# Optimization experiments

Measured on AMD Instinct MI355X. Metric: run time of the kernel, lower is better.

## Reference

```python
import jax, jax.numpy as jnp
import numpy as np

B, I, N = 1024, 128, 256
UNFOLDS = 6  # ode_solver_unfolds


def _sig(v, mu, sigma):
    # v: [B, D] -> [B, D, 1]; mu/sigma: [D, N] -> broadcast [B, D, N]
    return jax.nn.sigmoid(sigma * (v[..., None] - mu))


def setup_inputs() -> dict:
    key = jax.random.key(0)
    ks = jax.random.split(key, 12)
    u = lambda k, shape, lo, hi: jax.random.uniform(k, shape, jnp.float32, lo, hi)
    pm1 = lambda k, shape: (2.0 * jax.random.randint(k, shape, 0, 2) - 1.0).astype(jnp.float32)
    return {
        "inputs": jax.random.normal(ks[0], (B, I), jnp.float32),
        "state": jax.random.normal(ks[1], (B, N), jnp.float32) * 0.1,
        "input_w": jnp.ones((I,), jnp.float32),
        "input_b": jnp.zeros((I,), jnp.float32),
        "sensory_mu": u(ks[2], (I, N), 0.3, 0.8),
        "sensory_sigma": u(ks[3], (I, N), 3.0, 8.0),
        "sensory_W": u(ks[4], (I, N), 0.01, 1.0),
        "sensory_erev": pm1(ks[5], (I, N)),
        "mu": u(ks[6], (N, N), 0.3, 0.8),
        "sigma": u(ks[7], (N, N), 3.0, 8.0),
        "W": u(ks[8], (N, N), 0.01, 1.0),
        "erev": pm1(ks[9], (N, N)),
        "vleak": u(ks[10], (N,), -0.2, 0.2),
        "gleak": jnp.ones((N,), jnp.float32),   # gleak_init_min == gleak_init_max == 1.0
        "cm_t": jnp.full((N,), 0.5, jnp.float32),  # cm_init_min == cm_init_max == 0.5
    }


def reference(inputs, state, input_w, input_b, sensory_mu, sensory_sigma,
              sensory_W, sensory_erev, mu, sigma, W, erev, vleak, gleak, cm_t):
    # Affine input mapping
    x = inputs * input_w + input_b  # [B, I]
    # Sensory synapse activations (constant across unfolds)
    s_act = sensory_W * _sig(x, sensory_mu, sensory_sigma)  # [B, I, N]
    w_num_sensory = jnp.sum(s_act * sensory_erev, axis=1)   # [B, N]
    w_den_sensory = jnp.sum(s_act, axis=1)                  # [B, N]

    def step(v_pre, _):
        w_act = W * _sig(v_pre, mu, sigma)                  # [B, N, N]
        w_num = jnp.sum(w_act * erev, axis=1) + w_num_sensory
        w_den = jnp.sum(w_act, axis=1) + w_den_sensory
        numerator = cm_t * v_pre + gleak * vleak + w_num
        denominator = cm_t + gleak + w_den
        return numerator / denominator, None

    v_pre, _ = jax.lax.scan(step, state, None, length=UNFOLDS)
    # module returns (outputs, next_state) with outputs == next_state
    return v_pre
```

## Files before the change

### kernel.cpp

```cpp
#include <hip/hip_runtime.h>


#define LOG2E 1.44269504088896340f

constexpr int Bn = 1024;
constexpr int In = 128;
constexpr int Nn = 256;
constexpr int UNFOLDS = 6;

#if __has_builtin(__builtin_amdgcn_exp2f)
#define EXP2F(x) __builtin_amdgcn_exp2f(x)
#else
#define EXP2F(x) __exp2f(x)
#endif
#if __has_builtin(__builtin_amdgcn_rcpf)
#define RCPF(x) __builtin_amdgcn_rcpf(x)
#else
#define RCPF(x) (1.0f / (x))
#endif

__global__ __launch_bounds__(256) void pack_kernel(
    const float* __restrict__ mu, const float* __restrict__ sigma,
    const float* __restrict__ W, const float* __restrict__ erev,
    const float* __restrict__ smu, const float* __restrict__ ssigma,
    const float* __restrict__ sW, const float* __restrict__ serev,
    float4* __restrict__ Prec, float4* __restrict__ Psen) {
    int idx = blockIdx.x * 256 + threadIdx.x;
    if (idx < Nn * Nn) {
        float s = sigma[idx], m = mu[idx], w = W[idx], e = erev[idx];
        Prec[idx] = make_float4(s * LOG2E, s * m * LOG2E, w, w * e);
        return;
    }
    int j = idx - Nn * Nn;
    if (j < In * Nn) {
        float s = ssigma[j], m = smu[j], w = sW[j], e = serev[j];
        Psen[j] = make_float4(s * LOG2E, s * m * LOG2E, w, w * e);
    }
}

__global__ __launch_bounds__(1024, 1) void ltc_fused_kernel(
    const float* __restrict__ inputs, const float* __restrict__ state,
    const float* __restrict__ input_w, const float* __restrict__ input_b,
    const float4* __restrict__ Psen, const float4* __restrict__ Prec,
    const float* __restrict__ vleak, const float* __restrict__ gleak,
    const float* __restrict__ cmt, float* __restrict__ out) {
    __shared__ float4 vt[Nn];
    __shared__ float2 part[4][4][Nn];
    __shared__ float4 xs[In];

    const int tid = threadIdx.x;
    const int b0 = blockIdx.x * 4;
    const int n = tid & 255;
    const int ih = tid >> 8;

    float vp = state[(b0 + ih) * Nn + n];
    ((float*)vt)[n * 4 + ih] = vp;
    if (tid < 4 * In) {
        int i = tid & 127, bb = tid >> 7;
        ((float*)xs)[i * 4 + bb] =
            inputs[(b0 + bb) * In + i] * input_w[i] + input_b[i];
    }
    const float g = gleak[n], c = cmt[n];
    const float gvl = g * vleak[n];
    __syncthreads();

    float sens_n, sens_d;
    {
        float num[4] = {0.f, 0.f, 0.f, 0.f};
        float den[4] = {0.f, 0.f, 0.f, 0.f};
        const float4* __restrict__ pp = Psen + n;
#pragma unroll 8
        for (int i = ih * 32; i < ih * 32 + 32; ++i) {
            float4 p = pp[i * Nn];
            float4 v = xs[i];
#pragma unroll
            for (int bb = 0; bb < 4; ++bb) {
                float vb = (bb == 0) ? v.x : (bb == 1) ? v.y : (bb == 2) ? v.z : v.w;
                float r = RCPF(1.0f + EXP2F(fmaf(-p.x, vb, p.y)));
                den[bb] += p.z * r;
                num[bb] += p.w * r;
            }
        }
#pragma unroll
        for (int bb = 0; bb < 4; ++bb)
            part[ih][bb][n] = make_float2(num[bb], den[bb]);
        __syncthreads();
        float wn = 0.f, wd = 0.f;
#pragma unroll
        for (int s = 0; s < 4; ++s) {
            float2 v = part[s][ih][n];
            wn += v.x;
            wd += v.y;
        }
        sens_n = wn;
        sens_d = wd;
    }

    const float4* __restrict__ pp = Prec + n;
    for (int s = 0; s < UNFOLDS; ++s) {
        __syncthreads();
        float num[4] = {0.f, 0.f, 0.f, 0.f};
        float den[4] = {0.f, 0.f, 0.f, 0.f};
#pragma unroll 8
        for (int i = ih * 64; i < ih * 64 + 64; ++i) {
            float4 p = pp[i * Nn];
            float4 v = vt[i];
#pragma unroll
            for (int bb = 0; bb < 4; ++bb) {
                float vb = (bb == 0) ? v.x : (bb == 1) ? v.y : (bb == 2) ? v.z : v.w;
                float r = RCPF(1.0f + EXP2F(fmaf(-p.x, vb, p.y)));
                den[bb] += p.z * r;
                num[bb] += p.w * r;
            }
        }
#pragma unroll
        for (int bb = 0; bb < 4; ++bb)
            part[ih][bb][n] = make_float2(num[bb], den[bb]);
        __syncthreads();
        float wn = sens_n, wd = sens_d;
#pragma unroll
        for (int s2 = 0; s2 < 4; ++s2) {
            float2 v = part[s2][ih][n];
            wn += v.x;
            wd += v.y;
        }
        float res = (c * vp + gvl + wn) * RCPF(c + g + wd);
        vp = res;
        if (s == UNFOLDS - 1)
            out[(b0 + ih) * Nn + n] = res;
        else
            ((float*)vt)[n * 4 + ih] = res;
    }
}

extern "C" void kernel_launch(void* const* d_in, const int* in_sizes, int n_in,
                              void* d_out, int out_size, void* d_ws, size_t ws_size,
                              hipStream_t stream) {
    const float* inputs   = (const float*)d_in[0];
    const float* state    = (const float*)d_in[1];
    const float* input_w  = (const float*)d_in[2];
    const float* input_b  = (const float*)d_in[3];
    const float* smu      = (const float*)d_in[4];
    const float* ssigma   = (const float*)d_in[5];
    const float* sW       = (const float*)d_in[6];
    const float* serev    = (const float*)d_in[7];
    const float* mu       = (const float*)d_in[8];
    const float* sigma    = (const float*)d_in[9];
    const float* W        = (const float*)d_in[10];
    const float* erev     = (const float*)d_in[11];
    const float* vleak    = (const float*)d_in[12];
    const float* gleak    = (const float*)d_in[13];
    const float* cmt      = (const float*)d_in[14];
    float* out = (float*)d_out;

    char* ws = (char*)d_ws;
    float4* Prec = (float4*)ws;
    float4* Psen = (float4*)(ws + (1u << 20));

    pack_kernel<<<(Nn * Nn + In * Nn + 255) / 256, 256, 0, stream>>>(
        mu, sigma, W, erev, smu, ssigma, sW, serev, Prec, Psen);

    ltc_fused_kernel<<<Bn / 4, 1024, 0, stream>>>(
        inputs, state, input_w, input_b, Psen, Prec, vleak, gleak, cmt, out);
}
```

Baseline: 180.7 us.

## Split each batch group across two blocks with global-memory state exchange

Each group of 4 batch rows is now handled by a pair of blocks, each owning half of the 256 output neurons, which doubles the grid to 512 blocks so more of the GPU's compute units are busy. After every unfold the two blocks swap their updated state through a global buffer and sync on a per-pair atomic counter with spin-waiting. This adds inter-block dependencies that could deadlock if paired blocks are not resident together, which the spin bound only limits, and it adds global-memory round trips at each step. It also adds a memset launch.

```diff
diff --git a/kernel.cpp b/kernel.cpp
--- a/kernel.cpp
+++ b/kernel.cpp
@@ -38,39 +38,52 @@
     }
 }
 
-__global__ __launch_bounds__(1024, 1) void ltc_fused_kernel(
+__global__ __launch_bounds__(1024, 8) void ltc_fused_kernel(
     const float* __restrict__ inputs, const float* __restrict__ state,
     const float* __restrict__ input_w, const float* __restrict__ input_b,
     const float4* __restrict__ Psen, const float4* __restrict__ Prec,
     const float* __restrict__ vleak, const float* __restrict__ gleak,
-    const float* __restrict__ cmt, float* __restrict__ out) {
+    const float* __restrict__ cmt, float* __restrict__ out,
+    float* __restrict__ xchg, int* __restrict__ flags) {
     __shared__ float4 vt[Nn];
-    __shared__ float2 part[4][4][Nn];
     __shared__ float4 xs[In];
-
-    const int tid = threadIdx.x;
-    const int b0 = blockIdx.x * 4;
-    const int n = tid & 255;
-    const int ih = tid >> 8;
-
-    float vp = state[(b0 + ih) * Nn + n];
-    ((float*)vt)[n * 4 + ih] = vp;
-    if (tid < 4 * In) {
+    __shared__ float2 part[8][4][128];
+
+    const int tid    = threadIdx.x;
+    const int blk    = blockIdx.x;
+    const int pairid = blk >> 1;
+    const int nh     = blk & 1;
+    const int b0     = pairid * 4;
+    const int nl     = tid & 127;
+    const int ih     = tid >> 7;
+    const int ng     = (nh << 7) + nl;
+
+    {
+        int i = tid & 255, bb = tid >> 8;
+        ((float*)vt)[i * 4 + bb] = state[(b0 + bb) * Nn + i];
+    }
+    if (tid < 512) {
         int i = tid & 127, bb = tid >> 7;
         ((float*)xs)[i * 4 + bb] =
             inputs[(b0 + bb) * In + i] * input_w[i] + input_b[i];
     }
-    const float g = gleak[n], c = cmt[n];
-    const float gvl = g * vleak[n];
+    const bool is_red = (ih < 4);
+    float vp = 0.f, g = 0.f, c = 0.f, gvl = 0.f;
+    if (is_red) {
+        g   = gleak[ng];
+        c   = cmt[ng];
+        gvl = g * vleak[ng];
+    }
     __syncthreads();
-
-    float sens_n, sens_d;
+    if (is_red) vp = ((const float*)vt)[ng * 4 + ih];
+
+    float sens_n = 0.f, sens_d = 0.f;
     {
         float num[4] = {0.f, 0.f, 0.f, 0.f};
         float den[4] = {0.f, 0.f, 0.f, 0.f};
-        const float4* __restrict__ pp = Psen + n;
+        const float4* __restrict__ pp = Psen + ng;
 #pragma unroll 8
-        for (int i = ih * 32; i < ih * 32 + 32; ++i) {
+        for (int i = ih * 16; i < ih * 16 + 16; ++i) {
             float4 p = pp[i * Nn];
             float4 v = xs[i];
 #pragma unroll
@@ -83,26 +96,25 @@
         }
 #pragma unroll
         for (int bb = 0; bb < 4; ++bb)
-            part[ih][bb][n] = make_float2(num[bb], den[bb]);
+            part[ih][bb][nl] = make_float2(num[bb], den[bb]);
         __syncthreads();
-        float wn = 0.f, wd = 0.f;
-#pragma unroll
-        for (int s = 0; s < 4; ++s) {
-            float2 v = part[s][ih][n];
-            wn += v.x;
-            wd += v.y;
-        }
-        sens_n = wn;
-        sens_d = wd;
-    }
-
-    const float4* __restrict__ pp = Prec + n;
-    for (int s = 0; s < UNFOLDS; ++s) {
+        if (is_red) {
+#pragma unroll
+            for (int s = 0; s < 8; ++s) {
+                float2 v = part[s][ih][nl];
+                sens_n += v.x;
+                sens_d += v.y;
+            }
+        }
+    }
+
+    const float4* __restrict__ pp = Prec + ng;
+    for (int u = 0; u < UNFOLDS; ++u) {
         __syncthreads();
         float num[4] = {0.f, 0.f, 0.f, 0.f};
         float den[4] = {0.f, 0.f, 0.f, 0.f};
 #pragma unroll 8
-        for (int i = ih * 64; i < ih * 64 + 64; ++i) {
+        for (int i = ih * 32; i < ih * 32 + 32; ++i) {
             float4 p = pp[i * Nn];
             float4 v = vt[i];
 #pragma unroll
@@ -115,21 +127,50 @@
         }
 #pragma unroll
         for (int bb = 0; bb < 4; ++bb)
-            part[ih][bb][n] = make_float2(num[bb], den[bb]);
+            part[ih][bb][nl] = make_float2(num[bb], den[bb]);
         __syncthreads();
-        float wn = sens_n, wd = sens_d;
-#pragma unroll
-        for (int s2 = 0; s2 < 4; ++s2) {
-            float2 v = part[s2][ih][n];
-            wn += v.x;
-            wd += v.y;
-        }
-        float res = (c * vp + gvl + wn) * RCPF(c + g + wd);
-        vp = res;
-        if (s == UNFOLDS - 1)
-            out[(b0 + ih) * Nn + n] = res;
-        else
-            ((float*)vt)[n * 4 + ih] = res;
+
+        if (is_red) {
+            float wn = sens_n, wd = sens_d;
+#pragma unroll
+            for (int s = 0; s < 8; ++s) {
+                float2 v = part[s][ih][nl];
+                wn += v.x;
+                wd += v.y;
+            }
+            float res = (c * vp + gvl + wn) * RCPF(c + g + wd);
+            vp = res;
+            if (u == UNFOLDS - 1) {
+                out[(b0 + ih) * Nn + ng] = res;
+            } else {
+                ((float*)vt)[ng * 4 + ih] = res;
+                __hip_atomic_store(
+                    &xchg[(((u & 1) << 9) + blk) * 512 + (nl << 2) + ih], res,
+                    __ATOMIC_RELAXED, __HIP_MEMORY_SCOPE_AGENT);
+            }
+        }
+
+        if (u < UNFOLDS - 1) {
+            __syncthreads();
+            if (tid == 0) {
+                __hip_atomic_fetch_add(&flags[pairid], 1, __ATOMIC_RELAXED,
+                                       __HIP_MEMORY_SCOPE_AGENT);
+                const int target = 2 * (u + 1);
+                int it = 0;
+                while (__hip_atomic_load(&flags[pairid], __ATOMIC_RELAXED,
+                                         __HIP_MEMORY_SCOPE_AGENT) < target) {
+                    __builtin_amdgcn_s_sleep(2);
+                    if (++it > (1 << 20)) break;
+                }
+            }
+            __syncthreads();
+            if (tid < 512) {
+                float pv = __hip_atomic_load(
+                    &xchg[(((u & 1) << 9) + (blk ^ 1)) * 512 + tid],
+                    __ATOMIC_RELAXED, __HIP_MEMORY_SCOPE_AGENT);
+                ((float*)vt)[((1 - nh) << 9) + tid] = pv;
+            }
+        }
     }
 }
 
@@ -156,10 +197,15 @@
     char* ws = (char*)d_ws;
     float4* Prec = (float4*)ws;
     float4* Psen = (float4*)(ws + (1u << 20));
+    float*  xchg = (float*)(ws + (1u << 20) + (1u << 19));
+    int*    flags = (int*)(ws + (1u << 20) + (1u << 19) + (2u << 20));
+
+    hipMemsetAsync(flags, 0, 256 * sizeof(int), stream);
 
     pack_kernel<<<(Nn * Nn + In * Nn + 255) / 256, 256, 0, stream>>>(
         mu, sigma, W, erev, smu, ssigma, sW, serev, Prec, Psen);
 
-    ltc_fused_kernel<<<Bn / 4, 1024, 0, stream>>>(
-        inputs, state, input_w, input_b, Psen, Prec, vleak, gleak, cmt, out);
+    ltc_fused_kernel<<<dim3(Bn / 4 * 2), dim3(1024), 0, stream>>>(
+        inputs, state, input_w, input_b, Psen, Prec, vleak, gleak, cmt, out,
+        xchg, flags);
 }
```

Result: slower. 211.4 us (+17.0%).

## Pack W and W*erev as bf16 pair and use 2-batch blocks

Applied to the files above, without the earlier changes.

Stores the synapse weight and weight*erev pair as two bf16 halves in one 32-bit word, splitting the parameter layout into a float2 array for the sigmoid coefficients and a uint array for the weights. This cuts parameter bytes per synapse from 16 to 12. The fused kernel now processes 2 batch rows per 512-thread block with up to 4 blocks per CU instead of 4 rows per 1024-thread block. That raises block count and occupancy but halves the reuse of each loaded parameter across batch rows. Rounding the weights to bf16 introduces precision loss in the accumulated sums.

```diff
diff --git a/kernel.cpp b/kernel.cpp
--- a/kernel.cpp
+++ b/kernel.cpp
@@ -19,45 +19,57 @@
 #define RCPF(x) (1.0f / (x))
 #endif
 
+__device__ __forceinline__ unsigned int pack_bf16_pair(float w, float we) {
+    unsigned int uw = __float_as_uint(w);
+    unsigned int ue = __float_as_uint(we);
+    uw = (uw + 0x7fffu + ((uw >> 16) & 1u)) & 0xffff0000u;
+    ue = (ue + 0x7fffu + ((ue >> 16) & 1u)) >> 16;
+    return uw | ue;
+}
+
 __global__ __launch_bounds__(256) void pack_kernel(
     const float* __restrict__ mu, const float* __restrict__ sigma,
     const float* __restrict__ W, const float* __restrict__ erev,
     const float* __restrict__ smu, const float* __restrict__ ssigma,
     const float* __restrict__ sW, const float* __restrict__ serev,
-    float4* __restrict__ Prec, float4* __restrict__ Psen) {
+    float2* __restrict__ PAB, unsigned int* __restrict__ PWE,
+    float2* __restrict__ SAB, unsigned int* __restrict__ SWE) {
     int idx = blockIdx.x * 256 + threadIdx.x;
     if (idx < Nn * Nn) {
         float s = sigma[idx], m = mu[idx], w = W[idx], e = erev[idx];
-        Prec[idx] = make_float4(s * LOG2E, s * m * LOG2E, w, w * e);
+        PAB[idx] = make_float2(s * LOG2E, s * m * LOG2E);
+        PWE[idx] = pack_bf16_pair(w, w * e);
         return;
     }
     int j = idx - Nn * Nn;
     if (j < In * Nn) {
         float s = ssigma[j], m = smu[j], w = sW[j], e = serev[j];
-        Psen[j] = make_float4(s * LOG2E, s * m * LOG2E, w, w * e);
+        SAB[j] = make_float2(s * LOG2E, s * m * LOG2E);
+        SWE[j] = pack_bf16_pair(w, w * e);
     }
 }
 
-__global__ __launch_bounds__(1024, 1) void ltc_fused_kernel(
+__global__ __launch_bounds__(512, 4) void ltc_fused_kernel(
     const float* __restrict__ inputs, const float* __restrict__ state,
     const float* __restrict__ input_w, const float* __restrict__ input_b,
-    const float4* __restrict__ Psen, const float4* __restrict__ Prec,
+    const float2* __restrict__ SAB, const unsigned int* __restrict__ SWE,
+    const float2* __restrict__ PAB, const unsigned int* __restrict__ PWE,
     const float* __restrict__ vleak, const float* __restrict__ gleak,
     const float* __restrict__ cmt, float* __restrict__ out) {
-    __shared__ float4 vt[Nn];
-    __shared__ float2 part[4][4][Nn];
-    __shared__ float4 xs[In];
+    __shared__ float2 vt[Nn];
+    __shared__ float2 xs[In];
+    __shared__ float2 part[2][2][Nn];
 
     const int tid = threadIdx.x;
-    const int b0 = blockIdx.x * 4;
+    const int b0 = blockIdx.x * 2;
     const int n = tid & 255;
     const int ih = tid >> 8;
 
     float vp = state[(b0 + ih) * Nn + n];
-    ((float*)vt)[n * 4 + ih] = vp;
-    if (tid < 4 * In) {
+    ((float*)vt)[n * 2 + ih] = vp;
+    if (tid < 2 * In) {
         int i = tid & 127, bb = tid >> 7;
-        ((float*)xs)[i * 4 + bb] =
+        ((float*)xs)[i * 2 + bb] =
             inputs[(b0 + bb) * In + i] * input_w[i] + input_b[i];
     }
     const float g = gleak[n], c = cmt[n];
@@ -66,70 +78,58 @@
 
     float sens_n, sens_d;
     {
-        float num[4] = {0.f, 0.f, 0.f, 0.f};
-        float den[4] = {0.f, 0.f, 0.f, 0.f};
-        const float4* __restrict__ pp = Psen + n;
+        float num0 = 0.f, num1 = 0.f, den0 = 0.f, den1 = 0.f;
+        const float2* __restrict__ ab = SAB + n;
+        const unsigned int* __restrict__ we = SWE + n;
 #pragma unroll 8
-        for (int i = ih * 32; i < ih * 32 + 32; ++i) {
-            float4 p = pp[i * Nn];
-            float4 v = xs[i];
-#pragma unroll
-            for (int bb = 0; bb < 4; ++bb) {
-                float vb = (bb == 0) ? v.x : (bb == 1) ? v.y : (bb == 2) ? v.z : v.w;
-                float r = RCPF(1.0f + EXP2F(fmaf(-p.x, vb, p.y)));
-                den[bb] += p.z * r;
-                num[bb] += p.w * r;
-            }
+        for (int i = ih * 64; i < ih * 64 + 64; ++i) {
+            float2 p = ab[i * Nn];
+            unsigned int wp = we[i * Nn];
+            float2 v = xs[i];
+            float Wv  = __uint_as_float(wp & 0xffff0000u);
+            float Wev = __uint_as_float(wp << 16);
+            float r0 = RCPF(1.0f + EXP2F(fmaf(-p.x, v.x, p.y)));
+            float r1 = RCPF(1.0f + EXP2F(fmaf(-p.x, v.y, p.y)));
+            den0 += Wv * r0;  num0 += Wev * r0;
+            den1 += Wv * r1;  num1 += Wev * r1;
         }
-#pragma unroll
-        for (int bb = 0; bb < 4; ++bb)
-            part[ih][bb][n] = make_float2(num[bb], den[bb]);
+        part[ih][0][n] = make_float2(num0, den0);
+        part[ih][1][n] = make_float2(num1, den1);
         __syncthreads();
-        float wn = 0.f, wd = 0.f;
-#pragma unroll
-        for (int s = 0; s < 4; ++s) {
-            float2 v = part[s][ih][n];
-            wn += v.x;
-            wd += v.y;
-        }
-        sens_n = wn;
-        sens_d = wd;
+        float2 p0 = part[0][ih][n], p1 = part[1][ih][n];
+        sens_n = p0.x + p1.x;
+        sens_d = p0.y + p1.y;
     }
 
-    const float4* __restrict__ pp = Prec + n;
+    const float2* __restrict__ ab = PAB + n;
+    const unsigned int* __restrict__ wep = PWE + n;
     for (int s = 0; s < UNFOLDS; ++s) {
         __syncthreads();
-        float num[4] = {0.f, 0.f, 0.f, 0.f};
-        float den[4] = {0.f, 0.f, 0.f, 0.f};
+        float num0 = 0.f, num1 = 0.f, den0 = 0.f, den1 = 0.f;
 #pragma unroll 8
-        for (int i = ih * 64; i < ih * 64 + 64; ++i) {
-            float4 p = pp[i * Nn];
-            float4 v = vt[i];
-#pragma unroll
-            for (int bb = 0; bb < 4; ++bb) {
-                float vb = (bb == 0) ? v.x : (bb == 1) ? v.y : (bb == 2) ? v.z : v.w;
-                float r = RCPF(1.0f + EXP2F(fmaf(-p.x, vb, p.y)));
-                den[bb] += p.z * r;
-                num[bb] += p.w * r;
-            }
+        for (int i = ih * 128; i < ih * 128 + 128; ++i) {
+            float2 p = ab[i * Nn];
+            unsigned int wp = wep[i * Nn];
+            float2 v = vt[i];
+            float Wv  = __uint_as_float(wp & 0xffff0000u);
+            float Wev = __uint_as_float(wp << 16);
+            float r0 = RCPF(1.0f + EXP2F(fmaf(-p.x, v.x, p.y)));
+            float r1 = RCPF(1.0f + EXP2F(fmaf(-p.x, v.y, p.y)));
+            den0 += Wv * r0;  num0 += Wev * r0;
+            den1 += Wv * r1;  num1 += Wev * r1;
         }
-#pragma unroll
-        for (int bb = 0; bb < 4; ++bb)
-            part[ih][bb][n] = make_float2(num[bb], den[bb]);
+        part[ih][0][n] = make_float2(num0, den0);
+        part[ih][1][n] = make_float2(num1, den1);
         __syncthreads();
-        float wn = sens_n, wd = sens_d;
-#pragma unroll
-        for (int s2 = 0; s2 < 4; ++s2) {
-            float2 v = part[s2][ih][n];
-            wn += v.x;
-            wd += v.y;
-        }
+        float2 p0 = part[0][ih][n], p1 = part[1][ih][n];
+        float wn = sens_n + p0.x + p1.x;
+        float wd = sens_d + p0.y + p1.y;
         float res = (c * vp + gvl + wn) * RCPF(c + g + wd);
         vp = res;
         if (s == UNFOLDS - 1)
             out[(b0 + ih) * Nn + n] = res;
         else
-            ((float*)vt)[n * 4 + ih] = res;
+            ((float*)vt)[n * 2 + ih] = res;
     }
 }
 
@@ -154,12 +154,15 @@
     float* out = (float*)d_out;
 
     char* ws = (char*)d_ws;
-    float4* Prec = (float4*)ws;
-    float4* Psen = (float4*)(ws + (1u << 20));
+    float2*       PAB = (float2*)(ws);
+    unsigned int* PWE = (unsigned int*)(ws + (512u << 10));
+    float2*       SAB = (float2*)(ws + (768u << 10));
+    unsigned int* SWE = (unsigned int*)(ws + (1024u << 10));
 
     pack_kernel<<<(Nn * Nn + In * Nn + 255) / 256, 256, 0, stream>>>(
-        mu, sigma, W, erev, smu, ssigma, sW, serev, Prec, Psen);
+        mu, sigma, W, erev, smu, ssigma, sW, serev, PAB, PWE, SAB, SWE);
 
-    ltc_fused_kernel<<<Bn / 4, 1024, 0, stream>>>(
-        inputs, state, input_w, input_b, Psen, Prec, vleak, gleak, cmt, out);
+    ltc_fused_kernel<<<Bn / 2, 512, 0, stream>>>(
+        inputs, state, input_w, input_b, SAB, SWE, PAB, PWE,
+        vleak, gleak, cmt, out);
 }
```

New measurement: 254.2 us. 40.6% more time.

## Remap threads so the reduction uses wave shuffles and batch reciprocals

Applied to the files above, without the earlier changes.

Threads are remapped so the four partial-sum lanes for a neuron sit adjacent in a wave. The cross-partition reduction then uses butterfly shuffles instead of a shared-memory partial buffer and an extra barrier. State is double-buffered with padded indexing to avoid bank conflicts, leaving one barrier per unfold. In the recurrent loop four reciprocals are replaced by one reciprocal of a product plus multiplies, which trades transcendental throughput for extra FMAs and a risk of overflow when exponentials are large. Global loads of Prec are now less coalesced, because adjacent lanes read rows 64 apart.

```diff
diff --git a/kernel.cpp b/kernel.cpp
--- a/kernel.cpp
+++ b/kernel.cpp
@@ -44,20 +44,19 @@
     const float4* __restrict__ Psen, const float4* __restrict__ Prec,
     const float* __restrict__ vleak, const float* __restrict__ gleak,
     const float* __restrict__ cmt, float* __restrict__ out) {
-    __shared__ float4 vt[Nn];
-    __shared__ float2 part[4][4][Nn];
-    __shared__ float4 xs[In];
+    __shared__ float4 vt[2][260];
+    __shared__ float4 xs[132];
 
     const int tid = threadIdx.x;
     const int b0 = blockIdx.x * 4;
-    const int n = tid & 255;
-    const int ih = tid >> 8;
+    const int n  = tid >> 2;
+    const int ih = tid & 3;
 
     float vp = state[(b0 + ih) * Nn + n];
-    ((float*)vt)[n * 4 + ih] = vp;
-    if (tid < 4 * In) {
-        int i = tid & 127, bb = tid >> 7;
-        ((float*)xs)[i * 4 + bb] =
+    ((float*)vt[0])[((n + (n >> 6)) << 2) + ih] = vp;
+    if (tid < 512) {
+        int i = tid >> 2, bb = tid & 3;
+        ((float*)xs)[((i + (i >> 5)) << 2) + bb] =
             inputs[(b0 + bb) * In + i] * input_w[i] + input_b[i];
     }
     const float g = gleak[n], c = cmt[n];
@@ -66,70 +65,87 @@
 
     float sens_n, sens_d;
     {
-        float num[4] = {0.f, 0.f, 0.f, 0.f};
-        float den[4] = {0.f, 0.f, 0.f, 0.f};
+        float pn[4] = {0.f, 0.f, 0.f, 0.f};
+        float pd[4] = {0.f, 0.f, 0.f, 0.f};
         const float4* __restrict__ pp = Psen + n;
 #pragma unroll 8
-        for (int i = ih * 32; i < ih * 32 + 32; ++i) {
+        for (int ii = 0; ii < 32; ++ii) {
+            int i = ih * 32 + ii;
             float4 p = pp[i * Nn];
-            float4 v = xs[i];
-#pragma unroll
-            for (int bb = 0; bb < 4; ++bb) {
-                float vb = (bb == 0) ? v.x : (bb == 1) ? v.y : (bb == 2) ? v.z : v.w;
-                float r = RCPF(1.0f + EXP2F(fmaf(-p.x, vb, p.y)));
-                den[bb] += p.z * r;
-                num[bb] += p.w * r;
-            }
+            float4 v = xs[i + ih];
+            float r0 = RCPF(1.0f + EXP2F(fmaf(-p.x, v.x, p.y)));
+            float r1 = RCPF(1.0f + EXP2F(fmaf(-p.x, v.y, p.y)));
+            float r2 = RCPF(1.0f + EXP2F(fmaf(-p.x, v.z, p.y)));
+            float r3 = RCPF(1.0f + EXP2F(fmaf(-p.x, v.w, p.y)));
+            pd[0] += p.z * r0; pn[0] += p.w * r0;
+            pd[1] += p.z * r1; pn[1] += p.w * r1;
+            pd[2] += p.z * r2; pn[2] += p.w * r2;
+            pd[3] += p.z * r3; pn[3] += p.w * r3;
         }
-#pragma unroll
-        for (int bb = 0; bb < 4; ++bb)
-            part[ih][bb][n] = make_float2(num[bb], den[bb]);
-        __syncthreads();
-        float wn = 0.f, wd = 0.f;
-#pragma unroll
-        for (int s = 0; s < 4; ++s) {
-            float2 v = part[s][ih][n];
-            wn += v.x;
-            wd += v.y;
-        }
-        sens_n = wn;
-        sens_d = wd;
+        const bool hi = (ih & 2) != 0;
+        float sn0 = hi ? pn[0] : pn[2], sn1 = hi ? pn[1] : pn[3];
+        float sd0 = hi ? pd[0] : pd[2], sd1 = hi ? pd[1] : pd[3];
+        sn0 = __shfl_xor(sn0, 2); sn1 = __shfl_xor(sn1, 2);
+        sd0 = __shfl_xor(sd0, 2); sd1 = __shfl_xor(sd1, 2);
+        float an0 = (hi ? pn[2] : pn[0]) + sn0;
+        float an1 = (hi ? pn[3] : pn[1]) + sn1;
+        float ad0 = (hi ? pd[2] : pd[0]) + sd0;
+        float ad1 = (hi ? pd[3] : pd[1]) + sd1;
+        const bool odd = (ih & 1) != 0;
+        float sn = odd ? an0 : an1, sd = odd ? ad0 : ad1;
+        sn = __shfl_xor(sn, 1); sd = __shfl_xor(sd, 1);
+        sens_n = (odd ? an1 : an0) + sn;
+        sens_d = (odd ? ad1 : ad0) + sd;
     }
 
     const float4* __restrict__ pp = Prec + n;
+    int cur = 0;
     for (int s = 0; s < UNFOLDS; ++s) {
         __syncthreads();
-        float num[4] = {0.f, 0.f, 0.f, 0.f};
-        float den[4] = {0.f, 0.f, 0.f, 0.f};
+        float pn[4] = {0.f, 0.f, 0.f, 0.f};
+        float pd[4] = {0.f, 0.f, 0.f, 0.f};
+        const float4* __restrict__ vc = vt[cur];
 #pragma unroll 8
-        for (int i = ih * 64; i < ih * 64 + 64; ++i) {
+        for (int ii = 0; ii < 64; ++ii) {
+            int i = ih * 64 + ii;
             float4 p = pp[i * Nn];
-            float4 v = vt[i];
-#pragma unroll
-            for (int bb = 0; bb < 4; ++bb) {
-                float vb = (bb == 0) ? v.x : (bb == 1) ? v.y : (bb == 2) ? v.z : v.w;
-                float r = RCPF(1.0f + EXP2F(fmaf(-p.x, vb, p.y)));
-                den[bb] += p.z * r;
-                num[bb] += p.w * r;
-            }
+            float4 v = vc[i + ih];
+            float a0 = 1.0f + EXP2F(fmaf(-p.x, v.x, p.y));
+            float a1 = 1.0f + EXP2F(fmaf(-p.x, v.y, p.y));
+            float a2 = 1.0f + EXP2F(fmaf(-p.x, v.z, p.y));
+            float a3 = 1.0f + EXP2F(fmaf(-p.x, v.w, p.y));
+            float p01 = a0 * a1, p23 = a2 * a3;
+            float rp  = RCPF(p01 * p23);
+            float q01 = p23 * rp, q23 = p01 * rp;
+            float r0 = a1 * q01, r1 = a0 * q01;
+            float r2 = a3 * q23, r3 = a2 * q23;
+            pd[0] += p.z * r0; pn[0] += p.w * r0;
+            pd[1] += p.z * r1; pn[1] += p.w * r1;
+            pd[2] += p.z * r2; pn[2] += p.w * r2;
+            pd[3] += p.z * r3; pn[3] += p.w * r3;
         }
-#pragma unroll
-        for (int bb = 0; bb < 4; ++bb)
-            part[ih][bb][n] = make_float2(num[bb], den[bb]);
-        __syncthreads();
-        float wn = sens_n, wd = sens_d;
-#pragma unroll
-        for (int s2 = 0; s2 < 4; ++s2) {
-            float2 v = part[s2][ih][n];
-            wn += v.x;
-            wd += v.y;
-        }
+        const bool hi = (ih & 2) != 0;
+        float sn0 = hi ? pn[0] : pn[2], sn1 = hi ? pn[1] : pn[3];
+        float sd0 = hi ? pd[0] : pd[2], sd1 = hi ? pd[1] : pd[3];
+        sn0 = __shfl_xor(sn0, 2); sn1 = __shfl_xor(sn1, 2);
+        sd0 = __shfl_xor(sd0, 2); sd1 = __shfl_xor(sd1, 2);
+        float an0 = (hi ? pn[2] : pn[0]) + sn0;
+        float an1 = (hi ? pn[3] : pn[1]) + sn1;
+        float ad0 = (hi ? pd[2] : pd[0]) + sd0;
+        float ad1 = (hi ? pd[3] : pd[1]) + sd1;
+        const bool odd = (ih & 1) != 0;
+        float sn = odd ? an0 : an1, sd = odd ? ad0 : ad1;
+        sn = __shfl_xor(sn, 1); sd = __shfl_xor(sd, 1);
+        float wn = sens_n + (odd ? an1 : an0) + sn;
+        float wd = sens_d + (odd ? ad1 : ad0) + sd;
+
         float res = (c * vp + gvl + wn) * RCPF(c + g + wd);
         vp = res;
         if (s == UNFOLDS - 1)
             out[(b0 + ih) * Nn + n] = res;
         else
-            ((float*)vt)[n * 4 + ih] = res;
+            ((float*)vt[cur ^ 1])[((n + (n >> 6)) << 2) + ih] = res;
+        cur ^= 1;
     }
 }
 
```

After: 271.4 us. +50.2%, slower.
